# Kernel tuning notes

Measured on AMD Instinct MI355X. Metric: run time of the kernel, lower is better.

Reference implementation:

```python
import jax, jax.numpy as jnp
import numpy as np
from jax.scipy.special import gammaln

EPS = 1e-8
MAX_DISPERSION = 20.0

D, C, G, V, VG, GL = 200, 8, 10000, 20000, 50000, 500


def nb2_log_prob(mu, dispersion, value):
    # NegativeBinomial2: total_count = 1/dispersion, logits = log(mu+eps) - log(1/dispersion+eps)
    dispersion = jnp.minimum(dispersion, MAX_DISPERSION)
    total_count = 1.0 / dispersion
    logits = jnp.log(mu + EPS) - jnp.log(total_count + EPS)
    log_unnorm = total_count * jax.nn.log_sigmoid(-logits) + value * jax.nn.log_sigmoid(logits)
    log_norm = -gammaln(total_count + value) + gammaln(1.0 + value) + gammaln(total_count)
    return log_unnorm - log_norm


def setup_inputs() -> dict:
    key = jax.random.key(0)
    ks = jax.random.split(key, 9)
    fc_log = 0.1 * jax.random.normal(ks[0], (C, VG), dtype=jnp.float32)
    genotypes = jax.random.randint(ks[1], (D, V), 0, 3).astype(jnp.float32)
    expression_obs = jax.random.randint(ks[2], (D, C, GL), 0, 100).astype(jnp.float32)
    lib = 0.5 + 1.5 * jax.random.uniform(ks[3], (D, C), dtype=jnp.float32)
    baseline_log = jax.random.normal(ks[4], (C, G), dtype=jnp.float32)
    dispersion_log = jax.random.normal(ks[5], (C, G), dtype=jnp.float32)
    variantxgene_to_gene = jax.random.randint(ks[6], (VG,), 0, G)
    local_variant_to_local_variantxgene_selector = jax.random.randint(ks[7], (VG,), 0, V)
    variantxgene_to_local_gene = jax.random.randint(ks[8], (VG,), 0, GL)
    return {
        "fc_log": fc_log,
        "genotypes": genotypes,
        "expression_obs": expression_obs,
        "lib": lib,
        "baseline_log": baseline_log,
        "dispersion_log": dispersion_log,
        "variantxgene_to_gene": variantxgene_to_gene,
        "local_variant_to_local_variantxgene_selector": local_variant_to_local_variantxgene_selector,
        "variantxgene_to_local_gene": variantxgene_to_local_gene,
    }


def reference(fc_log, genotypes, expression_obs, lib, baseline_log, dispersion_log,
              variantxgene_to_gene, local_variant_to_local_variantxgene_selector,
              variantxgene_to_local_gene):
    # gather genotypes per variantxgene pair: (D, VG)
    g = genotypes[:, local_variant_to_local_variantxgene_selector]
    # expression delta: (D, C, VG)
    expression_delta = g[:, None, :] * fc_log[None, :, :]
    expression_log = baseline_log[:, variantxgene_to_gene][None, :, :] + expression_delta
    expressed = jnp.exp(expression_log) * lib[:, :, None]  # (D, C, VG)
    dispersion = jnp.exp(dispersion_log)[:, variantxgene_to_gene]  # (C, VG)
    obs = expression_obs[:, :, variantxgene_to_local_gene]  # (D, C, VG)
    elbo = -nb2_log_prob(expressed, dispersion[None, :, :], obs)
    return elbo
```

## Files before the change

### kernel.cpp

```cpp
#include <hip/hip_runtime.h>

#define Dn 200
#define Cn 8
#define Gn 10000
#define Vn 20000
#define VGn 50000
#define GLn 500
#define EPSf 1e-8f
#define ZSPLIT 8
#define CHUNK (Dn / ZSPLIT)

__device__ __forceinline__ float stirling_lg(float y) {
    float ly  = __logf(y);
    float iv  = __builtin_amdgcn_rcpf(y);
    float iv2 = iv * iv;
    float ser = iv * (0.08333333333333f + iv2 * (-0.00277777777778f + iv2 * 0.00079365079365f));
    return fmaf(y - 0.5f, ly, -y) + 0.91893853320467274f + ser;
}

__device__ __forceinline__ float lgamma_shift8(float x) {
    const float q = x * (x + 7.0f);
    const float p = (q * (q + 6.0f)) * ((q + 10.0f) * (q + 12.0f));
    return stirling_lg(x + 8.0f) - __logf(p);
}

__global__ __launch_bounds__(256, 4) void elbo_kernel(
    const float* __restrict__ fc_log,
    const float* __restrict__ genotypes,
    const float* __restrict__ obs,
    const float* __restrict__ lib,
    const float* __restrict__ baseline_log,
    const float* __restrict__ dispersion_log,
    const int* __restrict__ v2g,
    const int* __restrict__ lv_sel,
    const int* __restrict__ v2lg,
    float* __restrict__ out)
{
    __shared__ float s_ltab[128];
    __shared__ float s_loglib[Dn * Cn];

    const int tid = threadIdx.x;
    int vg = blockIdx.x * 256 + tid;
    const bool active = (vg < VGn);
    if (!active) vg = VGn - 1;

    if (tid < 128) s_ltab[tid] = lgamma_shift8(1.0f + (float)tid);
    for (int idx = tid; idx < Dn * Cn; idx += 256)
        s_loglib[idx] = __logf(lib[idx]);

    const int lv   = lv_sel[vg];
    const int lg   = v2lg[vg];
    const int gene = v2g[vg];

    float fc[Cn], bl[Cn], r_[Cn], K_[Cn], r2e[Cn];
    #pragma unroll
    for (int c = 0; c < Cn; ++c) {
        fc[c] = fc_log[c * VGn + vg];
        bl[c] = baseline_log[c * Gn + gene];
        const float dl   = dispersion_log[c * Gn + gene];
        const float disp = fminf(__expf(dl), 20.0f);
        const float r    = 1.0f / disp;
        r_[c]  = r;
        K_[c]  = lgamma_shift8(r) - r * __logf(r + EPSf);
        r2e[c] = r + 2.0f * EPSf;
    }
    __syncthreads();

    const int d0 = blockIdx.z * CHUNK;
    const float* gp  = genotypes + (size_t)d0 * Vn + lv;
    const float* op  = obs + (size_t)d0 * (Cn * GLn) + lg;
    float*       wp  = out + (size_t)d0 * (Cn * VGn) + vg;
    const float* llp = s_loglib + d0 * Cn;

    #pragma unroll 2
    for (int i = 0; i < CHUNK; ++i) {
        const float g = *gp; gp += Vn;

        float val[Cn];
        #pragma unroll
        for (int c = 0; c < Cn; ++c) val[c] = op[c * GLn];
        op += Cn * GLn;

        #pragma unroll
        for (int c = 0; c < Cn; ++c) {
            const float value = val[c];
            const float s  = fmaf(g, fc[c], bl[c] + llp[c]);
            const float mu = __expf(s);
            const float L  = __logf(r2e[c] + mu);
            const float rv = r_[c] + value;

            int vi = (int)value;
            vi = vi < 0 ? 0 : (vi > 127 ? 127 : vi);

            const float lgrv = lgamma_shift8(rv);
            const float e = fmaf(rv, L, K_[c]) - value * s + s_ltab[vi] - lgrv;
            if (active) wp[c * VGn] = e;
        }
        llp += Cn;
        wp  += Cn * VGn;
    }
}

extern "C" void kernel_launch(void* const* d_in, const int* in_sizes, int n_in,
                              void* d_out, int out_size, void* d_ws, size_t ws_size,
                              hipStream_t stream) {
    const float* fc_log         = (const float*)d_in[0];
    const float* genotypes      = (const float*)d_in[1];
    const float* obs            = (const float*)d_in[2];
    const float* lib            = (const float*)d_in[3];
    const float* baseline_log   = (const float*)d_in[4];
    const float* dispersion_log = (const float*)d_in[5];
    const int* v2g    = (const int*)d_in[6];
    const int* lv_sel = (const int*)d_in[7];
    const int* v2lg   = (const int*)d_in[8];
    float* out = (float*)d_out;

    dim3 grid((VGn + 255) / 256, 1, ZSPLIT);
    elbo_kernel<<<grid, 256, 0, stream>>>(fc_log, genotypes, obs, lib,
                                          baseline_log, dispersion_log,
                                          v2g, lv_sel, v2lg, out);
}
```

Before: 520.5 us.

## Stage obs rows in shared memory with register prefetch and interleave z-chunks

Each block now loads the full obs row for the current d (8x500 floats) coalesced via float4 into shared memory, with a register double-buffer prefetch of the next row and next genotype. Per-thread random gathers from global memory become LDS gathers. The grid is flattened so that consecutive blocks cover different d-chunks of the same vg tile, and log(lib) is computed only for the block's own chunk. The Stirling series is also shortened by one term, which trades accuracy for fewer ops, and two barriers per iteration are added.

Result: slower. 635.9 us (+22.2%).

```diff
diff --git a/kernel.cpp b/kernel.cpp
--- a/kernel.cpp
+++ b/kernel.cpp
@@ -9,12 +9,14 @@
 #define EPSf 1e-8f
 #define ZSPLIT 8
 #define CHUNK (Dn / ZSPLIT)
+#define OBS_ROW (Cn * GLn)
+#define OBS_VEC (OBS_ROW / 4)
 
 __device__ __forceinline__ float stirling_lg(float y) {
     float ly  = __logf(y);
     float iv  = __builtin_amdgcn_rcpf(y);
     float iv2 = iv * iv;
-    float ser = iv * (0.08333333333333f + iv2 * (-0.00277777777778f + iv2 * 0.00079365079365f));
+    float ser = iv * fmaf(iv2, -0.00277777777778f, 0.08333333333333f);
     return fmaf(y - 0.5f, ly, -y) + 0.91893853320467274f + ser;
 }
 
@@ -36,17 +38,22 @@
     const int* __restrict__ v2lg,
     float* __restrict__ out)
 {
+    __shared__ float s_obs[OBS_ROW];
     __shared__ float s_ltab[128];
-    __shared__ float s_loglib[Dn * Cn];
+    __shared__ float s_ll[CHUNK * Cn];
 
     const int tid = threadIdx.x;
-    int vg = blockIdx.x * 256 + tid;
+    const int id  = blockIdx.x;
+    const int z   = id & 7;
+    const int xb  = id >> 3;
+    int vg = xb * 256 + tid;
     const bool active = (vg < VGn);
     if (!active) vg = VGn - 1;
+    const int d0 = z * CHUNK;
 
     if (tid < 128) s_ltab[tid] = lgamma_shift8(1.0f + (float)tid);
-    for (int idx = tid; idx < Dn * Cn; idx += 256)
-        s_loglib[idx] = __logf(lib[idx]);
+    for (int idx = tid; idx < CHUNK * Cn; idx += 256)
+        s_ll[idx] = __logf(lib[d0 * Cn + idx]);
 
     const int lv   = lv_sel[vg];
     const int lg   = v2lg[vg];
@@ -64,26 +71,45 @@
         K_[c]  = lgamma_shift8(r) - r * __logf(r + EPSf);
         r2e[c] = r + 2.0f * EPSf;
     }
-    __syncthreads();
 
-    const int d0 = blockIdx.z * CHUNK;
-    const float* gp  = genotypes + (size_t)d0 * Vn + lv;
-    const float* op  = obs + (size_t)d0 * (Cn * GLn) + lg;
-    float*       wp  = out + (size_t)d0 * (Cn * VGn) + vg;
-    const float* llp = s_loglib + d0 * Cn;
+    const float* gp   = genotypes + (size_t)d0 * Vn + lv;
+    const float* orow = obs + (size_t)d0 * OBS_ROW;
+    float*       wp   = out + ((size_t)d0 * Cn) * VGn + vg;
 
-    #pragma unroll 2
+    float4 st[4];
+    #pragma unroll
+    for (int k = 0; k < 4; ++k) {
+        const int j = tid + 256 * k;
+        if (j < OBS_VEC) st[k] = reinterpret_cast<const float4*>(orow)[j];
+    }
+    float g = *gp;
+    gp += Vn;
+    orow += OBS_ROW;
+
     for (int i = 0; i < CHUNK; ++i) {
-        const float g = *gp; gp += Vn;
+        #pragma unroll
+        for (int k = 0; k < 4; ++k) {
+            const int j = tid + 256 * k;
+            if (j < OBS_VEC) reinterpret_cast<float4*>(s_obs)[j] = st[k];
+        }
+        __syncthreads();
 
-        float val[Cn];
-        #pragma unroll
-        for (int c = 0; c < Cn; ++c) val[c] = op[c * GLn];
-        op += Cn * GLn;
+        float gn = 0.0f;
+        if (i + 1 < CHUNK) {
+            #pragma unroll
+            for (int k = 0; k < 4; ++k) {
+                const int j = tid + 256 * k;
+                if (j < OBS_VEC) st[k] = reinterpret_cast<const float4*>(orow)[j];
+            }
+            gn = *gp;
+        }
+        gp += Vn;
+        orow += OBS_ROW;
 
+        const float* llp = s_ll + i * Cn;
         #pragma unroll
         for (int c = 0; c < Cn; ++c) {
-            const float value = val[c];
+            const float value = s_obs[c * GLn + lg];
             const float s  = fmaf(g, fc[c], bl[c] + llp[c]);
             const float mu = __expf(s);
             const float L  = __logf(r2e[c] + mu);
@@ -92,12 +118,12 @@
             int vi = (int)value;
             vi = vi < 0 ? 0 : (vi > 127 ? 127 : vi);
 
-            const float lgrv = lgamma_shift8(rv);
-            const float e = fmaf(rv, L, K_[c]) - value * s + s_ltab[vi] - lgrv;
-            if (active) wp[c * VGn] = e;
+            const float e = fmaf(rv, L, K_[c]) - value * s + s_ltab[vi] - lgamma_shift8(rv);
+            if (active) wp[(size_t)c * VGn] = e;
         }
-        llp += Cn;
-        wp  += Cn * VGn;
+        wp += (size_t)Cn * VGn;
+        g = gn;
+        __syncthreads();
     }
 }
 
@@ -115,7 +141,7 @@
     const int* v2lg   = (const int*)d_in[8];
     float* out = (float*)d_out;
 
-    dim3 grid((VGn + 255) / 256, 1, ZSPLIT);
+    dim3 grid(((VGn + 255) / 256) * ZSPLIT, 1, 1);
     elbo_kernel<<<grid, 256, 0, stream>>>(fc_log, genotypes, obs, lib,
                                           baseline_log, dispersion_log,
                                           v2g, lv_sel, v2lg, out);
```
